# Optimization experiments

Hardware: AMD Instinct MI355X
Metric: run time of the kernel (lower is better)

The kernel has to match this reference:

```python
import jax, jax.numpy as jnp
import numpy as np
import math

EPS = 1e-5

def _ln(x, g, b):
    m = jnp.mean(x, axis=-1, keepdims=True)
    v = jnp.var(x, axis=-1, keepdims=True)
    return (x - m) * jax.lax.rsqrt(v + EPS) * g + b

def _rn_layer(x, W, g, b, A, Bb, Rw):
    # x: (B,S,in) -> (B,S,out). W: (out,in), A: (out,basis), Bb: (basis,out)
    S = x.shape[1]
    basis_dim = Bb.shape[0]
    n = _ln(x @ W.T, g, b)                      # (B,S,out)
    j = jnp.arange(S) % basis_dim               # (S,)
    Bv = Bb[j]                                  # (S,out)
    scal = jnp.einsum('bsd,sd->bs', n, Bv)      # (B,S)
    Av = A[:, j].T                              # (S,out)
    nf = scal[..., None] * Av                   # (B,S,out)
    res = x if Rw is None else x @ Rw.T
    return nf + res

def _ts_layer(x, M, g, b, P, Rw):
    # x: (B,S,in) -> (B,S,out). M: (out,in), P: (out,out,G)
    S = x.shape[1]
    D, _, G = P.shape
    t = _ln(x @ M.T, g, b)                      # (B,S,out)
    k = jnp.arange(S, dtype=jnp.float32)
    periods = (jnp.arange(D, dtype=jnp.float32)[:, None, None] * (D * G)
               + jnp.arange(D, dtype=jnp.float32)[None, :, None] * G
               + jnp.arange(G, dtype=jnp.float32)[None, None, :] + 2.0)  # (D,D,G)
    phi = jnp.cos(2.0 * math.pi * k[:, None, None, None] / periods)       # (S,D,D,G)
    # Nk[b,s,i] = sum_{j,g} P[i,j,g] * t[b,s,j] * phi[s,i,j,g]
    Wp = jnp.einsum('ijg,sijg->sij', P, phi)    # (S,D,D)
    Nk = jnp.einsum('sij,bsj->bsi', Wp, t)      # (B,S,D)
    return Nk + x @ Rw.T

def setup_inputs() -> dict:
    key = jax.random.key(0)
    ks = jax.random.split(key, 16)
    B, S = 2, 2048
    d0, d1, d2 = 512, 64, 512        # input_dim, ts out, final out
    bas1, G, bas3 = 64, 8, 64
    u = lambda k, sh, a: jax.random.uniform(k, sh, jnp.float32, -a, a)
    inp = {
        'x':  jax.random.normal(ks[0], (B, S, d0), jnp.float32),
        # Layer 1: RN 512->512 (in==out -> no residual proj)
        'W1': u(ks[1], (d0, d0), 0.1),
        'g1': jnp.ones((d0,), jnp.float32),
        'b1': jnp.zeros((d0,), jnp.float32),
        'A1': u(ks[2], (d0, bas1), 0.1),
        'B1': u(ks[3], (bas1, d0), 0.1),
        # Layer 2: TS 512->64
        'M2': u(ks[4], (d1, d0), 0.5),
        'g2': jnp.ones((d1,), jnp.float32),
        'b2': jnp.zeros((d1,), jnp.float32),
        'P2': u(ks[5], (d1, d1, G), 0.1),
        'R2': u(ks[6], (d1, d0), 0.1),
        # Layer 3: RN 64->512
        'W3': u(ks[7], (d2, d1), 0.1),
        'g3': jnp.ones((d2,), jnp.float32),
        'b3': jnp.zeros((d2,), jnp.float32),
        'A3': u(ks[8], (d2, bas3), 0.1),
        'B3': u(ks[9], (bas3, d2), 0.1),
        'R3': u(ks[10], (d2, d1), 0.1),
    }
    return inp

def reference(x, W1, g1, b1, A1, B1, M2, g2, b2, P2, R2, W3, g3, b3, A3, B3, R3):
    h = _rn_layer(x, W1, g1, b1, A1, B1, None)   # (B,S,512), identity residual
    h = _ts_layer(h, M2, g2, b2, P2, R2)         # (B,S,64)
    h = _rn_layer(h, W3, g3, b3, A3, B3, R3)     # (B,S,512)
    return h
```

## Files before the change

### kernel.cpp

```cpp
#include <hip/hip_runtime.h>
#include <math.h>

#define SEQ  2048
#define ROWS 4096
#define D0   512
#define D1   64

typedef short bf8 __attribute__((ext_vector_type(8)));
typedef float f4  __attribute__((ext_vector_type(4)));

__device__ __forceinline__ unsigned short f2bf(float f) {
    unsigned u = __float_as_uint(f);
    return (unsigned short)((u + 0x7fffu + ((u >> 16) & 1u)) >> 16);
}
__device__ __forceinline__ void hilo(float f, unsigned short& h, unsigned short& l) {
    h = f2bf(f);
    float fh = __uint_as_float((unsigned)h << 16);
    l = f2bf(f - fh);
}
__device__ __forceinline__ void cv4(unsigned short* dh, unsigned short* dl, int idx, float4 v) {
    ushort4 hv, lv;
    hilo(v.x, hv.x, lv.x); hilo(v.y, hv.y, lv.y);
    hilo(v.z, hv.z, lv.z); hilo(v.w, hv.w, lv.w);
    *(ushort4*)(dh + idx) = hv;
    *(ushort4*)(dl + idx) = lv;
}

__device__ __forceinline__ void async16(const void* g, void* l) {
    __builtin_amdgcn_global_load_lds(
        (const __attribute__((address_space(1))) unsigned int*)g,
        (__attribute__((address_space(3))) unsigned int*)l, 16, 0, 0);
}

__global__ __launch_bounds__(256) void convk(
        const float* __restrict__ x,  const float* __restrict__ W1,
        const float* __restrict__ M2, const float* __restrict__ R2,
        const float* __restrict__ W3, const float* __restrict__ R3,
        const float* __restrict__ A1, const float* __restrict__ A3,
        unsigned short* __restrict__ xh,  unsigned short* __restrict__ xl,
        unsigned short* __restrict__ W1h, unsigned short* __restrict__ W1l,
        unsigned short* __restrict__ C2h, unsigned short* __restrict__ C2l,
        unsigned short* __restrict__ C3h, unsigned short* __restrict__ C3l,
        float* __restrict__ A1T, float* __restrict__ A3T) {
    int c = blockIdx.x, tid = threadIdx.x;
    if (c < 1216) {
        const float* src; unsigned short *dh, *dl; int off;
        if      (c < 1024) { src = x;  dh = xh;          dl = xl;          off = c; }
        else if (c < 1152) { src = W1; dh = W1h;         dl = W1l;         off = c - 1024; }
        else if (c < 1168) { src = M2; dh = C2h;         dl = C2l;         off = c - 1152; }
        else if (c < 1184) { src = R2; dh = C2h + 32768; dl = C2l + 32768; off = c - 1168; }
        else if (c < 1200) { src = W3; dh = C3h;         dl = C3l;         off = c - 1184; }
        else               { src = R3; dh = C3h + 32768; dl = C3l + 32768; off = c - 1200; }
        int base = off * 2048 + tid * 4;
        cv4(dh, dl, base,        *(const float4*)(src + base));
        cv4(dh, dl, base + 1024, *(const float4*)(src + base + 1024));
    } else {
        int gid = (c - 1216) * 256 + tid;
        int i = gid >> 6, j = gid & 63;
        A1T[j * 512 + i] = A1[gid];
        A3T[j * 512 + i] = A3[gid];
    }
}

__global__ __launch_bounds__(256, 4) void gemm64(
        const unsigned short* __restrict__ Ah, const unsigned short* __restrict__ Al,
        const unsigned short* __restrict__ Wh, const unsigned short* __restrict__ Wl,
        float* __restrict__ C, int M, int N, int K, int Ks) {
    __shared__ __align__(16) unsigned short aH[4096], aL[4096], wH[4096], wL[4096];
    const int tid = threadIdx.x;
    const int wv  = tid >> 6;
    const int ln  = tid & 63;
    const int lm  = ln & 15;
    const int lq  = ln >> 4;
    const int bm  = blockIdx.y * 64;
    const int bn  = blockIdx.x * 64;
    const int k0  = blockIdx.z * Ks;
    C += (size_t)blockIdx.z * M * N;

    f4 acc[4] = {};

    for (int kt = 0; kt < Ks; kt += 64) {
        const int kg = k0 + kt;
        __syncthreads();
#pragma unroll
        for (int i = 0; i < 2; ++i) {
            int slot = i * 256 + wv * 64 + ln;
            int row  = slot >> 3;
            int ch   = (slot & 7) ^ (row & 7);
            size_t goA = (size_t)(bm + row) * K + kg + ch * 8;
            size_t goW = (size_t)(bn + row) * K + kg + ch * 8;
            async16(Ah + goA, aH + slot * 8);
            async16(Al + goA, aL + slot * 8);
            async16(Wh + goW, wH + slot * 8);
            async16(Wl + goW, wL + slot * 8);
        }
        __syncthreads();

#pragma unroll
        for (int kk = 0; kk < 2; ++kk) {
            const int ck = kk * 4 + lq;
            const int r  = wv * 16 + lm;
            bf8 ah = *(const bf8*)(aH + r * 64 + ((ck ^ (r & 7)) * 8));
            bf8 al = *(const bf8*)(aL + r * 64 + ((ck ^ (r & 7)) * 8));
            bf8 bh[4], bl[4];
#pragma unroll
            for (int u = 0; u < 4; ++u) {
                int rb = u * 16 + lm;
                bh[u] = *(const bf8*)(wH + rb * 64 + ((ck ^ (rb & 7)) * 8));
                bl[u] = *(const bf8*)(wL + rb * 64 + ((ck ^ (rb & 7)) * 8));
            }
#pragma unroll
            for (int u = 0; u < 4; ++u) {
                acc[u] = __builtin_amdgcn_mfma_f32_16x16x32_bf16(ah, bh[u], acc[u], 0, 0, 0);
                acc[u] = __builtin_amdgcn_mfma_f32_16x16x32_bf16(ah, bl[u], acc[u], 0, 0, 0);
                acc[u] = __builtin_amdgcn_mfma_f32_16x16x32_bf16(al, bh[u], acc[u], 0, 0, 0);
            }
        }
    }

#pragma unroll
    for (int u = 0; u < 4; ++u) {
        int row = bm + wv * 16 + lq * 4;
        int col = bn + u * 16 + lm;
#pragma unroll
        for (int r = 0; r < 4; ++r)
            C[(size_t)(row + r) * N + col] = acc[u][r];
    }
}

__global__ __launch_bounds__(256) void lnrn(
        const float* __restrict__ Y, const float* __restrict__ Y2, int ldy,
        const float* __restrict__ RES, int ldr,
        const float* __restrict__ g, const float* __restrict__ be,
        const float* __restrict__ Bb, const float* __restrict__ AaT,
        float* __restrict__ outf,
        unsigned short* __restrict__ outh, unsigned short* __restrict__ outl) {
    const int row = blockIdx.x * 4 + (threadIdx.x >> 6);
    const int l = threadIdx.x & 63;
    const int c = l * 8;
    const float* y = Y + (size_t)row * ldy + c;
    float4 y0 = *(const float4*)y;
    float4 y1 = *(const float4*)(y + 4);
    if (Y2) {
        const float* y2 = Y2 + (size_t)row * ldy + c;
        float4 p0 = *(const float4*)y2, p1 = *(const float4*)(y2 + 4);
        y0.x += p0.x; y0.y += p0.y; y0.z += p0.z; y0.w += p0.w;
        y1.x += p1.x; y1.y += p1.y; y1.z += p1.z; y1.w += p1.w;
    }
    float sum = y0.x + y0.y + y0.z + y0.w + y1.x + y1.y + y1.z + y1.w;
    float ssq = y0.x*y0.x + y0.y*y0.y + y0.z*y0.z + y0.w*y0.w
              + y1.x*y1.x + y1.y*y1.y + y1.z*y1.z + y1.w*y1.w;
#pragma unroll
    for (int m = 1; m < 64; m <<= 1) {
        sum += __shfl_xor(sum, m, 64);
        ssq += __shfl_xor(ssq, m, 64);
    }
    float mean = sum * (1.0f / 512.0f);
    float var  = ssq * (1.0f / 512.0f) - mean * mean;
    float rstd = rsqrtf(var + 1e-5f);
    float4 g0 = *(const float4*)(g + c),  g1v = *(const float4*)(g + c + 4);
    float4 e0 = *(const float4*)(be + c), e1  = *(const float4*)(be + c + 4);
    float4 n0, n1;
    n0.x = (y0.x - mean) * rstd * g0.x  + e0.x;
    n0.y = (y0.y - mean) * rstd * g0.y  + e0.y;
    n0.z = (y0.z - mean) * rstd * g0.z  + e0.z;
    n0.w = (y0.w - mean) * rstd * g0.w  + e0.w;
    n1.x = (y1.x - mean) * rstd * g1v.x + e1.x;
    n1.y = (y1.y - mean) * rstd * g1v.y + e1.y;
    n1.z = (y1.z - mean) * rstd * g1v.z + e1.z;
    n1.w = (y1.w - mean) * rstd * g1v.w + e1.w;
    const int jm = row & 63;
    const float* bb = Bb + jm * D0 + c;
    float4 b0 = *(const float4*)bb, b1v = *(const float4*)(bb + 4);
    float p = n0.x*b0.x + n0.y*b0.y + n0.z*b0.z + n0.w*b0.w
            + n1.x*b1v.x + n1.y*b1v.y + n1.z*b1v.z + n1.w*b1v.w;
#pragma unroll
    for (int m = 1; m < 64; m <<= 1) p += __shfl_xor(p, m, 64);
    const float* av = AaT + jm * D0 + c;
    float4 a0 = *(const float4*)av, a1 = *(const float4*)(av + 4);
    const float* rs = RES + (size_t)row * ldr + c;
    float4 r0 = *(const float4*)rs, r1 = *(const float4*)(rs + 4);
    float4 v0, v1;
    v0.x = p*a0.x + r0.x; v0.y = p*a0.y + r0.y; v0.z = p*a0.z + r0.z; v0.w = p*a0.w + r0.w;
    v1.x = p*a1.x + r1.x; v1.y = p*a1.y + r1.y; v1.z = p*a1.z + r1.z; v1.w = p*a1.w + r1.w;
    if (outf) {
        *(float4*)(outf + (size_t)row * D0 + c)     = v0;
        *(float4*)(outf + (size_t)row * D0 + c + 4) = v1;
    } else {
        ushort4 h0, l0, h1, l1;
        hilo(v0.x, h0.x, l0.x); hilo(v0.y, h0.y, l0.y);
        hilo(v0.z, h0.z, l0.z); hilo(v0.w, h0.w, l0.w);
        hilo(v1.x, h1.x, l1.x); hilo(v1.y, h1.y, l1.y);
        hilo(v1.z, h1.z, l1.z); hilo(v1.w, h1.w, l1.w);
        *(ushort4*)(outh + (size_t)row * D0 + c)     = h0;
        *(ushort4*)(outl + (size_t)row * D0 + c)     = l0;
        *(ushort4*)(outh + (size_t)row * D0 + c + 4) = h1;
        *(ushort4*)(outl + (size_t)row * D0 + c + 4) = l1;
    }
}

#define C2S 524288
__global__ __launch_bounds__(256, 8) void tsk(
        const float* __restrict__ C2, const float* __restrict__ g2,
        const float* __restrict__ b2, const float* __restrict__ P,
        unsigned short* __restrict__ Hh, unsigned short* __restrict__ Hl) {
    __shared__ float tsh[2][64];
    __shared__ float rsh[2][64];
    __shared__ float part[4][2][64];
    const int s = blockIdx.x;
    const int tid = threadIdx.x;

    if (tid < 128) {
        int b = tid >> 6, j = tid & 63;
        size_t bs = (size_t)(b * SEQ + s) * 128;
        float v = 0.f, rv = 0.f;
#pragma unroll
        for (int z = 0; z < 8; ++z) {
            v  += C2[(size_t)z * C2S + bs + j];
            rv += C2[(size_t)z * C2S + bs + 64 + j];
        }
        rsh[b][j] = rv;
        float sum = v, ssq = v * v;
#pragma unroll
        for (int m = 1; m < 64; m <<= 1) {
            sum += __shfl_xor(sum, m, 64);
            ssq += __shfl_xor(ssq, m, 64);
        }
        float mean = sum * (1.0f / 64.0f);
        float var  = ssq * (1.0f / 64.0f) - mean * mean;
        float rstd = rsqrtf(var + 1e-5f);
        tsh[b][j] = (v - mean) * rstd * g2[j] + b2[j];
    }
    __syncthreads();

    const int i  = tid & 63;
    const int jg = tid >> 6;
    const float sf = (float)s;
    float a0 = 0.f, a1 = 0.f;
    for (int jj = 0; jj < 16; ++jj) {
        int j = (jg << 4) + jj;
        const float* pp = P + (i * 64 + j) * 8;
        float base = (float)(i * 512 + j * 8 + 2);
        float w = 0.f;
#pragma unroll
        for (int gg = 0; gg < 8; ++gg) {
            float pval = base + (float)gg;
            float invp = __builtin_amdgcn_rcpf(pval);
            float q    = floorf(sf * invp);
            float rem  = fmaf(-q, pval, sf);
            float fr   = rem * invp;
            fr = fr - floorf(fr);
            float cc = __builtin_amdgcn_cosf(fr);
            w = fmaf(pp[gg], cc, w);
        }
        a0 = fmaf(w, tsh[0][j], a0);
        a1 = fmaf(w, tsh[1][j], a1);
    }
    part[jg][0][i] = a0;
    part[jg][1][i] = a1;
    __syncthreads();

    if (tid < 128) {
        int b = tid >> 6, ii = tid & 63;
        float nk = part[0][b][ii] + part[1][b][ii] + part[2][b][ii] + part[3][b][ii]
                 + rsh[b][ii];
        size_t idx = (size_t)(b * SEQ + s) * D1 + ii;
        unsigned short h, lo_;
        hilo(nk, h, lo_);
        Hh[idx] = h; Hl[idx] = lo_;
    }
}

extern "C" void kernel_launch(void* const* d_in, const int* in_sizes, int n_in,
                              void* d_out, int out_size, void* d_ws, size_t ws_size,
                              hipStream_t stream) {
    const float* x  = (const float*)d_in[0];
    const float* W1 = (const float*)d_in[1];
    const float* g1 = (const float*)d_in[2];
    const float* b1 = (const float*)d_in[3];
    const float* A1 = (const float*)d_in[4];
    const float* B1 = (const float*)d_in[5];
    const float* M2 = (const float*)d_in[6];
    const float* g2 = (const float*)d_in[7];
    const float* b2 = (const float*)d_in[8];
    const float* P2 = (const float*)d_in[9];
    const float* R2 = (const float*)d_in[10];
    const float* W3 = (const float*)d_in[11];
    const float* g3 = (const float*)d_in[12];
    const float* b3 = (const float*)d_in[13];
    const float* A3 = (const float*)d_in[14];
    const float* B3 = (const float*)d_in[15];
    const float* R3 = (const float*)d_in[16];

    float* ws = (float*)d_ws;
    float* C1  = ws;
    float* C2  = ws + 4194304;
    float* C3  = ws + 8388608;
    float* A1T = ws + 12582912;
    float* A3T = ws + 12615680;
    unsigned short* us = (unsigned short*)(ws + 12648448);
    unsigned short* xh   = us;
    unsigned short* xl   = us + 2097152;
    unsigned short* h1h  = us + 4194304;
    unsigned short* h1l  = us + 6291456;
    unsigned short* W1h  = us + 8388608;
    unsigned short* W1l  = us + 8650752;
    unsigned short* Wc2h = us + 8912896;
    unsigned short* Wc2l = us + 8978432;
    unsigned short* Wc3h = us + 9043968;
    unsigned short* Wc3l = us + 9109504;
    unsigned short* h2h  = us + 9175040;
    unsigned short* h2l  = us + 9437184;

    dim3 blk(256);

    convk<<<1344, blk, 0, stream>>>(x, W1, M2, R2, W3, R3, A1, A3,
                                    xh, xl, W1h, W1l, Wc2h, Wc2l, Wc3h, Wc3l,
                                    A1T, A3T);

    gemm64<<<dim3(8, 64, 2), blk, 0, stream>>>(xh, xl, W1h, W1l, C1, ROWS, 512, 512, 256);
    lnrn<<<1024, blk, 0, stream>>>(C1, C1 + 2097152, 512, x, 512, g1, b1, B1, A1T,
                                   nullptr, h1h, h1l);

    gemm64<<<dim3(2, 64, 8), blk, 0, stream>>>(h1h, h1l, Wc2h, Wc2l, C2, ROWS, 128, 512, 64);
    tsk<<<SEQ, blk, 0, stream>>>(C2, g2, b2, P2, h2h, h2l);

    gemm64<<<dim3(16, 64, 1), blk, 0, stream>>>(h2h, h2l, Wc3h, Wc3l, C3, ROWS, 1024, 64, 64);
    lnrn<<<1024, blk, 0, stream>>>(C3, nullptr, 1024, C3 + 512, 1024, g3, b3, B3, A3T,
                                   (float*)d_out, nullptr, nullptr);
}
```

Measured before the change: 167.7 us.

## Replace per-step cosine evaluation with Chebyshev recurrence in time-series layer

The time-series kernel is split in two. A LayerNorm kernel writes normalized t and the residual sums. A new kernel assigns one (i,j) pair per lane and walks 64 consecutive sequence steps, producing the cosines with the recurrence cos((k+1)x)=2cos(x)cos(kx)-cos((k-1)x) instead of a range reduction and cos per element, then reduces over j with wave shuffles. The split-K count of the preceding GEMM is halved to four slices. This removes most transcendental work, but it adds an extra launch, shuffle-heavy reductions, and possible float drift from running the recurrence over 64 steps.

```diff
diff --git a/kernel.cpp b/kernel.cpp
--- a/kernel.cpp
+++ b/kernel.cpp
@@ -200,74 +200,110 @@
 }
 
 #define C2S 524288
-__global__ __launch_bounds__(256, 8) void tsk(
+__global__ __launch_bounds__(256) void lnt(
         const float* __restrict__ C2, const float* __restrict__ g2,
-        const float* __restrict__ b2, const float* __restrict__ P,
+        const float* __restrict__ b2,
+        float* __restrict__ t, float* __restrict__ rsum) {
+    const int r = blockIdx.x * 4 + (threadIdx.x >> 6);
+    const int j = threadIdx.x & 63;
+    size_t base = (size_t)r * 128 + j;
+    float v = 0.f, rv = 0.f;
+#pragma unroll
+    for (int z = 0; z < 4; ++z) {
+        v  += C2[(size_t)z * C2S + base];
+        rv += C2[(size_t)z * C2S + base + 64];
+    }
+    float sum = v, ssq = v * v;
+#pragma unroll
+    for (int m = 1; m < 64; m <<= 1) {
+        sum += __shfl_xor(sum, m, 64);
+        ssq += __shfl_xor(ssq, m, 64);
+    }
+    float mean = sum * (1.0f / 64.0f);
+    float var  = ssq * (1.0f / 64.0f) - mean * mean;
+    float rstd = rsqrtf(var + 1e-5f);
+    t[r * 64 + j]    = (v - mean) * rstd * g2[j] + b2[j];
+    rsum[r * 64 + j] = rv;
+}
+
+__global__ __launch_bounds__(256) void tsk2(
+        const float* __restrict__ t, const float* __restrict__ rsum,
+        const float* __restrict__ P,
         unsigned short* __restrict__ Hh, unsigned short* __restrict__ Hl) {
-    __shared__ float tsh[2][64];
-    __shared__ float rsh[2][64];
-    __shared__ float part[4][2][64];
-    const int s = blockIdx.x;
-    const int tid = threadIdx.x;
-
-    if (tid < 128) {
-        int b = tid >> 6, j = tid & 63;
-        size_t bs = (size_t)(b * SEQ + s) * 128;
-        float v = 0.f, rv = 0.f;
-#pragma unroll
-        for (int z = 0; z < 8; ++z) {
-            v  += C2[(size_t)z * C2S + bs + j];
-            rv += C2[(size_t)z * C2S + bs + 64 + j];
+    const int bid = blockIdx.x;
+    const int i   = bid >> 3;
+    const int sg  = bid & 7;
+    const int w   = threadIdx.x >> 6;
+    const int ln  = threadIdx.x & 63;
+    const int s0  = sg * 256 + w * 64;
+    const int idx = i * 64 + ln;
+    const float* pp = P + idx * 8;
+    const float sf0 = (float)s0;
+
+    float k2c[8], ca[8], cb[8];
+#pragma unroll
+    for (int g = 0; g < 8; ++g) {
+        float pf   = (float)(idx * 8 + g + 2);
+        float invp = __builtin_amdgcn_rcpf(pf);
+        k2c[g] = 2.0f * __builtin_amdgcn_cosf(invp);
+        float q0 = floorf(sf0 * invp);
+        float r0 = fmaf(-q0, pf, sf0);
+        float f0 = r0 * invp; f0 -= floorf(f0);
+        float c0 = __builtin_amdgcn_cosf(f0);
+        float sf1 = sf0 + 1.0f;
+        float q1 = floorf(sf1 * invp);
+        float r1 = fmaf(-q1, pf, sf1);
+        float f1 = r1 * invp; f1 -= floorf(f1);
+        float c1 = __builtin_amdgcn_cosf(f1);
+        float Pv = pp[g];
+        ca[g] = Pv * c0;
+        cb[g] = Pv * c1;
+    }
+
+    const int tb = s0 * 64 + ln;
+    float t0c = t[tb], t1c = t[131072 + tb];
+    float res0 = 0.f, res1 = 0.f;
+
+    for (int st = 0; st < 64; st += 2) {
+        float t0n  = t[tb + (st + 1) * 64];
+        float t1n  = t[131072 + tb + (st + 1) * 64];
+        float ws = ((ca[0] + ca[1]) + (ca[2] + ca[3]))
+                 + ((ca[4] + ca[5]) + (ca[6] + ca[7]));
+#pragma unroll
+        for (int g = 0; g < 8; ++g) ca[g] = fmaf(k2c[g], cb[g], -ca[g]);
+        float v0 = ws * t0c, v1 = ws * t1c;
+#pragma unroll
+        for (int m = 1; m < 64; m <<= 1) {
+            v0 += __shfl_xor(v0, m, 64);
+            v1 += __shfl_xor(v1, m, 64);
         }
-        rsh[b][j] = rv;
-        float sum = v, ssq = v * v;
+        res0 = (ln == st) ? v0 : res0;
+        res1 = (ln == st) ? v1 : res1;
+        float t0n2 = t[tb + (st + 2) * 64];
+        float t1n2 = t[131072 + tb + (st + 2) * 64];
+        float ws2 = ((cb[0] + cb[1]) + (cb[2] + cb[3]))
+                  + ((cb[4] + cb[5]) + (cb[6] + cb[7]));
+#pragma unroll
+        for (int g = 0; g < 8; ++g) cb[g] = fmaf(k2c[g], ca[g], -cb[g]);
+        float v0b = ws2 * t0n, v1b = ws2 * t1n;
 #pragma unroll
         for (int m = 1; m < 64; m <<= 1) {
-            sum += __shfl_xor(sum, m, 64);
-            ssq += __shfl_xor(ssq, m, 64);
+            v0b += __shfl_xor(v0b, m, 64);
+            v1b += __shfl_xor(v1b, m, 64);
         }
-        float mean = sum * (1.0f / 64.0f);
-        float var  = ssq * (1.0f / 64.0f) - mean * mean;
-        float rstd = rsqrtf(var + 1e-5f);
-        tsh[b][j] = (v - mean) * rstd * g2[j] + b2[j];
-    }
-    __syncthreads();
-
-    const int i  = tid & 63;
-    const int jg = tid >> 6;
-    const float sf = (float)s;
-    float a0 = 0.f, a1 = 0.f;
-    for (int jj = 0; jj < 16; ++jj) {
-        int j = (jg << 4) + jj;
-        const float* pp = P + (i * 64 + j) * 8;
-        float base = (float)(i * 512 + j * 8 + 2);
-        float w = 0.f;
-#pragma unroll
-        for (int gg = 0; gg < 8; ++gg) {
-            float pval = base + (float)gg;
-            float invp = __builtin_amdgcn_rcpf(pval);
-            float q    = floorf(sf * invp);
-            float rem  = fmaf(-q, pval, sf);
-            float fr   = rem * invp;
-            fr = fr - floorf(fr);
-            float cc = __builtin_amdgcn_cosf(fr);
-            w = fmaf(pp[gg], cc, w);
-        }
-        a0 = fmaf(w, tsh[0][j], a0);
-        a1 = fmaf(w, tsh[1][j], a1);
-    }
-    part[jg][0][i] = a0;
-    part[jg][1][i] = a1;
-    __syncthreads();
-
-    if (tid < 128) {
-        int b = tid >> 6, ii = tid & 63;
-        float nk = part[0][b][ii] + part[1][b][ii] + part[2][b][ii] + part[3][b][ii]
-                 + rsh[b][ii];
-        size_t idx = (size_t)(b * SEQ + s) * D1 + ii;
-        unsigned short h, lo_;
-        hilo(nk, h, lo_);
-        Hh[idx] = h; Hl[idx] = lo_;
+        res0 = (ln == st + 1) ? v0b : res0;
+        res1 = (ln == st + 1) ? v1b : res1;
+        t0c = t0n2; t1c = t1n2;
+    }
+
+    const int s = s0 + ln;
+    {
+        float v = res0 + rsum[(size_t)s * 64 + i];
+        unsigned short h, l; hilo(v, h, l);
+        Hh[(size_t)s * 64 + i] = h; Hl[(size_t)s * 64 + i] = l;
+        float v1e = res1 + rsum[(size_t)(SEQ + s) * 64 + i];
+        hilo(v1e, h, l);
+        Hh[(size_t)(SEQ + s) * 64 + i] = h; Hl[(size_t)(SEQ + s) * 64 + i] = l;
     }
 }
 
@@ -293,12 +329,14 @@
     const float* R3 = (const float*)d_in[16];
 
     float* ws = (float*)d_ws;
-    float* C1  = ws;
-    float* C2  = ws + 4194304;
-    float* C3  = ws + 8388608;
-    float* A1T = ws + 12582912;
-    float* A3T = ws + 12615680;
-    unsigned short* us = (unsigned short*)(ws + 12648448);
+    float* C1   = ws;
+    float* C2   = ws + 4194304;
+    float* C3   = ws + 6291456;
+    float* t    = ws + 10485760;
+    float* rsum = ws + 10747904;
+    float* A1T  = ws + 11010048;
+    float* A3T  = ws + 11042816;
+    unsigned short* us = (unsigned short*)(ws + 11075584);
     unsigned short* xh   = us;
     unsigned short* xl   = us + 2097152;
     unsigned short* h1h  = us + 4194304;
@@ -322,8 +360,9 @@
     lnrn<<<1024, blk, 0, stream>>>(C1, C1 + 2097152, 512, x, 512, g1, b1, B1, A1T,
                                    nullptr, h1h, h1l);
 
-    gemm64<<<dim3(2, 64, 8), blk, 0, stream>>>(h1h, h1l, Wc2h, Wc2l, C2, ROWS, 128, 512, 64);
-    tsk<<<SEQ, blk, 0, stream>>>(C2, g2, b2, P2, h2h, h2l);
+    gemm64<<<dim3(2, 64, 4), blk, 0, stream>>>(h1h, h1l, Wc2h, Wc2l, C2, ROWS, 128, 512, 128);
+    lnt<<<1024, blk, 0, stream>>>(C2, g2, b2, t, rsum);
+    tsk2<<<512, blk, 0, stream>>>(t, rsum, P2, h2h, h2l);
 
     gemm64<<<dim3(16, 64, 1), blk, 0, stream>>>(h2h, h2l, Wc3h, Wc3l, C3, ROWS, 1024, 64, 64);
     lnrn<<<1024, blk, 0, stream>>>(C3, nullptr, 1024, C3 + 512, 1024, g3, b3, B3, A3T,
```

Result: faster. 159.1 us (-5.1%).
